# Kernel tuning notes

Measured on AMD Instinct MI355X. Metric: run time of the kernel, lower is better.

The kernel has to match this reference:

```python
import jax, jax.numpy as jnp
import numpy as np

B, S, D = 32, 2048, 64
DK, DV = 24, 32

def setup_inputs() -> dict:
    key = jax.random.key(0)
    ks = jax.random.split(key, 5)
    # PyTorch nn.Linear(in,out) weight is [out,in]; we store transposed [in,out]
    # so y = x @ W matches x @ weight.T. Kaiming-uniform-ish scale.
    def init(k, fan_in, shape):
        bound = 1.0 / np.sqrt(fan_in)
        return jax.random.uniform(k, shape, jnp.float32, -bound, bound)
    return {
        "x": jax.random.normal(ks[0], (B, S, D), jnp.float32),
        "Wq": init(ks[1], D, (D, DK)),
        "Wk": init(ks[2], D, (D, DK)),
        "Wv": init(ks[3], D, (D, DV)),
        "Wh": init(ks[4], DV, (DV, D)),
    }

def reference(x, Wq, Wk, Wv, Wh):
    # x: [B,S,64]
    q = jnp.einsum("bsd,dk->bsk", x, Wq)          # [B,S,24]
    k = jnp.einsum("bsd,dk->bsk", x, Wk)          # [B,S,24]
    v = jnp.einsum("bsd,dk->bsk", x, Wv)          # [B,S,32]
    a = jnp.einsum("bqk,btk->bqt", q, k)          # [B,S,S], q @ k^T
    # NOTE: softmax over dim=1 (the query axis), as in the original module.
    a = jax.nn.softmax(a, axis=1)
    h1 = jnp.einsum("bqt,btv->bqv", a, v)         # [B,S,32]
    return jnp.einsum("bqv,vd->bqd", h1, Wh)      # [B,S,64]
```

## Files before the change

kernel.cpp:

```cpp
#include <hip/hip_runtime.h>
#include <hip/hip_bf16.h>

#define NB 32
#define NS 2048
#define ND 64
#define NDK 24
#define NDV 32
#define LOG2E 1.4426950408889634f

typedef __attribute__((ext_vector_type(8))) short short8;
typedef __attribute__((ext_vector_type(4))) float f32x4;

typedef __attribute__((address_space(3))) unsigned int lds_u32;
typedef __attribute__((address_space(1))) const unsigned int glb_u32;

#define LFENCE asm volatile("" ::: "memory")

__device__ __forceinline__ void cp16(const void* g, void* l) {
  __builtin_amdgcn_global_load_lds((glb_u32*)g, (lds_u32*)l, 16, 0, 0);
}

__device__ __forceinline__ float fexp2(float x) {
  return __builtin_amdgcn_exp2f(x);
}

__device__ __forceinline__ unsigned pk2(float a, float b) {
  __hip_bfloat16 ha = __float2bfloat16(a), hb = __float2bfloat16(b);
  return ((unsigned)__builtin_bit_cast(unsigned short, hb) << 16) |
         (unsigned)__builtin_bit_cast(unsigned short, ha);
}

__device__ __forceinline__ unsigned pku(__hip_bfloat16 lo, __hip_bfloat16 hi) {
  return ((unsigned)__builtin_bit_cast(unsigned short, hi) << 16) |
         (unsigned)__builtin_bit_cast(unsigned short, lo);
}


__global__ __launch_bounds__(256) void prep_kernel(
    const float* __restrict__ Wq, const float* __restrict__ Wk,
    const float* __restrict__ Wv, const float* __restrict__ Wh,
    __hip_bfloat16* __restrict__ wt, __hip_bfloat16* __restrict__ whT) {
  const int tid = threadIdx.x;
  for (int o = tid; o < 6144; o += 256) {
    const int n = o / 72, d = o % 72;
    float val = 0.f;
    if (o < 5760 && d < ND) {
      if (n < 24)      val = Wq[d * NDK + n] * LOG2E;
      else if (n < 48) val = Wk[d * NDK + (n - 24)];
      else             val = Wv[d * NDV + (n - 48)];
    }
    wt[o] = __float2bfloat16(val);
  }
  {
    const int lane = tid & 63, l15 = lane & 15, lg = lane >> 4;
    const int d = (tid >> 6) * 16 + l15;
    uint4 u;
    u.x = pk2(Wh[(lg * 8 + 0) * ND + d], Wh[(lg * 8 + 1) * ND + d]);
    u.y = pk2(Wh[(lg * 8 + 2) * ND + d], Wh[(lg * 8 + 3) * ND + d]);
    u.z = pk2(Wh[(lg * 8 + 4) * ND + d], Wh[(lg * 8 + 5) * ND + d]);
    u.w = pk2(Wh[(lg * 8 + 6) * ND + d], Wh[(lg * 8 + 7) * ND + d]);
    ((uint4*)whT)[tid] = u;
  }
}

__global__ __launch_bounds__(256) void proj_kernel(
    const float* __restrict__ x, const __hip_bfloat16* __restrict__ wt,
    __hip_bfloat16* __restrict__ qfb, __hip_bfloat16* __restrict__ kfb,
    __hip_bfloat16* __restrict__ vfb) {
  __shared__ __hip_bfloat16 xsb[64 * 72];
  __shared__ __hip_bfloat16 Wt[6144];
  __shared__ __hip_bfloat16 os[64][81];

  const int tid = threadIdx.x;
  const size_t row0 = (size_t)blockIdx.x * 64;
  const int b = (int)(row0 >> 11);
  const int tile = (int)((row0 >> 6) & 31);
  const int wv = tid >> 6, lane = tid & 63;
  const int l15 = lane & 15, lg = lane >> 4;

  #pragma unroll
  for (int i = 0; i < 3; ++i)
    cp16((const char*)wt + (i * 256 + tid) * 16, (char*)Wt + (i * 256 + tid) * 16);

  {
    const int r = tid >> 2, c16 = (tid & 3) * 16;
    const float4* src = (const float4*)(x + (row0 + r) * ND + c16);
    unsigned u[8];
    #pragma unroll
    for (int i = 0; i < 4; ++i) {
      float4 f = src[i];
      u[2 * i] = pk2(f.x, f.y);
      u[2 * i + 1] = pk2(f.z, f.w);
    }
    uint4* dst = (uint4*)((char*)xsb + r * 144 + c16 * 2);
    dst[0] = make_uint4(u[0], u[1], u[2], u[3]);
    dst[1] = make_uint4(u[4], u[5], u[6], u[7]);
  }
  __syncthreads();

  {
    short8 a[2];
    #pragma unroll
    for (int kc = 0; kc < 2; ++kc)
      a[kc] = *(const short8*)((char*)xsb + ((wv * 16 + l15) * 72 + kc * 32 + lg * 8) * 2);
    const f32x4 z = {0.f, 0.f, 0.f, 0.f};
    #pragma unroll
    for (int nt = 0; nt < 5; ++nt) {
      f32x4 acc = z;
      #pragma unroll
      for (int kc = 0; kc < 2; ++kc) {
        const short8 bfr = *(const short8*)((char*)Wt + ((nt * 16 + l15) * 72 + kc * 32 + lg * 8) * 2);
        acc = __builtin_amdgcn_mfma_f32_16x16x32_bf16(a[kc], bfr, acc, 0, 0, 0);
      }
      #pragma unroll
      for (int r = 0; r < 4; ++r)
        os[wv * 16 + lg * 4 + r][nt * 16 + l15] = __float2bfloat16(acc[r]);
    }
  }
  __syncthreads();

  const size_t fbase = ((size_t)(b * 32 + tile)) * 4 * 256;
  for (int j = tid; j < 2048; j += 256) {
    const int arr = j >> 10, jj = j & 1023;
    const int qs = jj >> 8, ln = (jj >> 2) & 63, wd = jj & 3;
    const int row = qs * 16 + (ln & 15);
    const int c0 = (ln >> 4) * 8 + wd * 2;
    unsigned u = 0;
    if (c0 < 24) u = pku(os[row][arr * 24 + c0], os[row][arr * 24 + c0 + 1]);
    unsigned* dst = (unsigned*)(arr ? kfb : qfb);
    dst[fbase + (size_t)qs * 256 + ln * 4 + wd] = u;
  }
  for (int j = tid; j < 1024; j += 256) {
    const int fi = j >> 8;
    const int ln = (j >> 2) & 63, wd = j & 3;
    const int v = (fi & 1) * 16 + (ln & 15);
    const int tl = (fi >> 1) * 32 + (ln >> 4) * 8 + wd * 2;
    const unsigned u = pku(os[tl][48 + v], os[tl + 1][48 + v]);
    ((unsigned*)vfb)[fbase + (size_t)fi * 256 + ln * 4 + wd] = u;
  }
}

struct QT { short8 q0, q1, q2, q3; };

__device__ __forceinline__ void loadQ(QT& t, const __hip_bfloat16* qp, int it, int lane) {
  const __hip_bfloat16* p = qp + (size_t)it * 2048 + lane * 8;
  t.q0 = *(const short8*)(p);
  t.q1 = *(const short8*)(p + 512);
  t.q2 = *(const short8*)(p + 1024);
  t.q3 = *(const short8*)(p + 1536);
}

__device__ __forceinline__ void accQ(const QT& t, short8 kf0, short8 kf1,
                                     f32x4& s0, f32x4& s1) {
  const f32x4 z = {0.f, 0.f, 0.f, 0.f};
  #pragma unroll
  for (int qi = 0; qi < 4; ++qi) {
    const short8 q = qi == 0 ? t.q0 : qi == 1 ? t.q1 : qi == 2 ? t.q2 : t.q3;
    f32x4 d0 = __builtin_amdgcn_mfma_f32_16x16x32_bf16(kf0, q, z, 0, 0, 0);
    f32x4 d1 = __builtin_amdgcn_mfma_f32_16x16x32_bf16(kf1, q, z, 0, 0, 0);
    #pragma unroll
    for (int r = 0; r < 4; ++r) { s0[r] += fexp2(d0[r]); s1[r] += fexp2(d1[r]); }
  }
}

__global__ __launch_bounds__(256) void stats_kernel(
    const __hip_bfloat16* __restrict__ qfb, const __hip_bfloat16* __restrict__ kfb,
    float* __restrict__ ls) {
  const int g = blockIdx.x;
  const int xcd = g & 7, loc = g >> 3;
  const int b = (xcd << 2) + (loc >> 4);
  const int tg = loc & 15;
  const int tid = threadIdx.x;
  const int wv = tid >> 6, lane = tid & 63;
  const int l15 = lane & 15, lg = lane >> 4;
  const int tile_t = tg * 2 + (wv >> 1);
  const int ib = (wv & 1) * 2;

  short8 kf[2];
  #pragma unroll
  for (int j = 0; j < 2; ++j)
    kf[j] = *(const short8*)(kfb + (((size_t)(b * 32 + tile_t)) * 4 + ib + j) * 512 + lane * 8);

  const __hip_bfloat16* qp = qfb + (size_t)b * 32 * 2048;
  const f32x4 z = {0.f, 0.f, 0.f, 0.f};
  f32x4 s0 = z, s1 = z;

  QT A, B;
  loadQ(A, qp, 0, lane);
  for (int it2 = 0; it2 < 16; ++it2) {
    const int itA = it2 * 2;
    loadQ(B, qp, itA + 1, lane);
    accQ(A, kf[0], kf[1], s0, s1);
    loadQ(A, qp, itA + 2 < 32 ? itA + 2 : 31, lane);
    accQ(B, kf[0], kf[1], s0, s1);
  }
  #pragma unroll
  for (int m = 1; m < 16; m <<= 1) {
    #pragma unroll
    for (int r = 0; r < 4; ++r) {
      s0[r] += __shfl_xor(s0[r], m);
      s1[r] += __shfl_xor(s1[r], m);
    }
  }
  if (l15 == 0) {
    f32x4 o0, o1;
    #pragma unroll
    for (int r = 0; r < 4; ++r) { o0[r] = -__log2f(s0[r]); o1[r] = -__log2f(s1[r]); }
    float* lp = ls + ((size_t)b << 11) + tile_t * 64 + ib * 16 + lg * 4;
    *(f32x4*)(lp) = o0;
    *(f32x4*)(lp + 16) = o1;
  }
}

struct KVT {
  short8 k0, k1, k2, k3;
  short8 v0, v1, v2, v3;
  f32x4 l0, l1, l2, l3;
};

__device__ __forceinline__ void loadKV(KVT& t, const __hip_bfloat16* kp0,
    const __hip_bfloat16* vp0, const float* lsb, int it, int lane, int lg) {
  const __hip_bfloat16* kp = kp0 + (size_t)it * 2048 + lane * 8;
  t.k0 = *(const short8*)(kp);
  t.k1 = *(const short8*)(kp + 512);
  t.k2 = *(const short8*)(kp + 1024);
  t.k3 = *(const short8*)(kp + 1536);
  const __hip_bfloat16* vp = vp0 + (size_t)it * 2048 + lane * 8;
  t.v0 = *(const short8*)(vp);
  t.v1 = *(const short8*)(vp + 512);
  t.v2 = *(const short8*)(vp + 1024);
  t.v3 = *(const short8*)(vp + 1536);
  const float* lp = lsb + it * 64 + lg * 4;
  t.l0 = *(const f32x4*)(lp);
  t.l1 = *(const f32x4*)(lp + 16);
  t.l2 = *(const f32x4*)(lp + 32);
  t.l3 = *(const f32x4*)(lp + 48);
}

__device__ __forceinline__ void computeKV(const KVT& t, short8 qf, char* Pw,
                                          int lg, f32x4& h10, f32x4& h11) {
  f32x4 d;
  uint2 w;
  d = __builtin_amdgcn_mfma_f32_16x16x32_bf16(t.k0, qf, t.l0, 0, 0, 0);
  w.x = pk2(fexp2(d[0]), fexp2(d[1]));
  w.y = pk2(fexp2(d[2]), fexp2(d[3]));
  *(uint2*)(Pw + lg * 8) = w;
  d = __builtin_amdgcn_mfma_f32_16x16x32_bf16(t.k1, qf, t.l1, 0, 0, 0);
  w.x = pk2(fexp2(d[0]), fexp2(d[1]));
  w.y = pk2(fexp2(d[2]), fexp2(d[3]));
  *(uint2*)(Pw + 32 + lg * 8) = w;
  d = __builtin_amdgcn_mfma_f32_16x16x32_bf16(t.k2, qf, t.l2, 0, 0, 0);
  w.x = pk2(fexp2(d[0]), fexp2(d[1]));
  w.y = pk2(fexp2(d[2]), fexp2(d[3]));
  *(uint2*)(Pw + 64 + lg * 8) = w;
  d = __builtin_amdgcn_mfma_f32_16x16x32_bf16(t.k3, qf, t.l3, 0, 0, 0);
  w.x = pk2(fexp2(d[0]), fexp2(d[1]));
  w.y = pk2(fexp2(d[2]), fexp2(d[3]));
  *(uint2*)(Pw + 96 + lg * 8) = w;
  LFENCE;
  const short8 p0 = *(const short8*)(Pw + lg * 16);
  const short8 p1 = *(const short8*)(Pw + 64 + lg * 16);
  h10 = __builtin_amdgcn_mfma_f32_16x16x32_bf16(p0, t.v0, h10, 0, 0, 0);
  h11 = __builtin_amdgcn_mfma_f32_16x16x32_bf16(p0, t.v1, h11, 0, 0, 0);
  h10 = __builtin_amdgcn_mfma_f32_16x16x32_bf16(p1, t.v2, h10, 0, 0, 0);
  h11 = __builtin_amdgcn_mfma_f32_16x16x32_bf16(p1, t.v3, h11, 0, 0, 0);
  LFENCE;
}

__global__ __launch_bounds__(256) void attn_kernel(
    const __hip_bfloat16* __restrict__ qfb, const __hip_bfloat16* __restrict__ kfb,
    const __hip_bfloat16* __restrict__ vfb, const float* __restrict__ ls,
    const __hip_bfloat16* __restrict__ whT, float* __restrict__ out) {
  __shared__ char Ps[4 * 2816];

  const int g = blockIdx.x;
  const int xcd = g & 7, loc = g >> 3;
  const int b = (xcd << 2) + (loc >> 4);
  const int qg = loc & 15;
  const int tid = threadIdx.x;
  const int wv = tid >> 6, lane = tid & 63;
  const int l15 = lane & 15, lg = lane >> 4;
  const int tile_q = qg * 2 + (wv >> 1);
  const int ib = (wv & 1) * 2;

  char* Pw = Ps + wv * 2816 + l15 * 176;

  short8 qf[2];
  #pragma unroll
  for (int qi = 0; qi < 2; ++qi)
    qf[qi] = *(const short8*)(qfb + (((size_t)(b * 32 + tile_q)) * 4 + ib + qi) * 512 + lane * 8);

  const __hip_bfloat16* kp0 = kfb + (size_t)b * 32 * 2048;
  const __hip_bfloat16* vp0 = vfb + (size_t)b * 32 * 2048;
  const float* lsb = ls + ((size_t)b << 11);

  const f32x4 z = {0.f, 0.f, 0.f, 0.f};
  f32x4 h1[2][2] = {{z, z}, {z, z}};

  KVT A, B;
  loadKV(A, kp0, vp0, lsb, 0, lane, lg);
  for (int it2 = 0; it2 < 16; ++it2) {
    const int itA = it2 * 2;
    loadKV(B, kp0, vp0, lsb, itA + 1, lane, lg);
    computeKV(A, qf[0], Pw, lg, h1[0][0], h1[0][1]);
    computeKV(A, qf[1], Pw, lg, h1[1][0], h1[1][1]);
    loadKV(A, kp0, vp0, lsb, itA + 2 < 32 ? itA + 2 : 31, lane, lg);
    computeKV(B, qf[0], Pw, lg, h1[0][0], h1[0][1]);
    computeKV(B, qf[1], Pw, lg, h1[1][0], h1[1][1]);
  }

  short8 wf[4];
  #pragma unroll
  for (int dt = 0; dt < 4; ++dt)
    wf[dt] = *(const short8*)(whT + dt * 512 + lane * 8);
  #pragma unroll
  for (int qi = 0; qi < 2; ++qi) {
    #pragma unroll
    for (int vs = 0; vs < 2; ++vs)
      #pragma unroll
      for (int r = 0; r < 4; ++r)
        *(unsigned short*)(Ps + wv * 2816 + (lg * 4 + r) * 176 + (vs * 16 + l15) * 2) =
            __builtin_bit_cast(unsigned short, __float2bfloat16(h1[qi][vs][r]));
    LFENCE;
    const short8 hf = *(const short8*)(Pw + lg * 16);
    float* ob = out + (size_t)(b * NS + tile_q * 64 + (ib + qi) * 16 + lg * 4) * ND + l15;
    #pragma unroll
    for (int dt = 0; dt < 4; ++dt) {
      f32x4 o = __builtin_amdgcn_mfma_f32_16x16x32_bf16(hf, wf[dt], z, 0, 0, 0);
      float* op = ob + dt * 16;
      op[0] = o[0];
      op[ND] = o[1];
      op[2 * ND] = o[2];
      op[3 * ND] = o[3];
    }
    LFENCE;
  }
}

extern "C" void kernel_launch(void* const* d_in, const int* in_sizes, int n_in,
                              void* d_out, int out_size, void* d_ws, size_t ws_size,
                              hipStream_t stream) {
  const float* x  = (const float*)d_in[0];
  const float* Wq = (const float*)d_in[1];
  const float* Wk = (const float*)d_in[2];
  const float* Wv = (const float*)d_in[3];
  const float* Wh = (const float*)d_in[4];
  float* out = (float*)d_out;

  char* ws = (char*)d_ws;
  __hip_bfloat16* qfb = (__hip_bfloat16*)ws;
  __hip_bfloat16* kfb = (__hip_bfloat16*)(ws + 4194304);
  __hip_bfloat16* vfb = (__hip_bfloat16*)(ws + 8388608);
  float*          lsp = (float*)(ws + 12582912);
  __hip_bfloat16* whT = (__hip_bfloat16*)(ws + 12845056);
  __hip_bfloat16* wt  = (__hip_bfloat16*)(ws + 12849152);

  hipLaunchKernelGGL(prep_kernel, dim3(1), dim3(256), 0, stream,
                     Wq, Wk, Wv, Wh, wt, whT);
  hipLaunchKernelGGL(proj_kernel, dim3(1024), dim3(256), 0, stream,
                     x, wt, qfb, kfb, vfb);
  hipLaunchKernelGGL(stats_kernel, dim3(512), dim3(256), 0, stream,
                     qfb, kfb, lsp);
  hipLaunchKernelGGL(attn_kernel, dim3(512), dim3(256), 0, stream,
                     qfb, kfb, vfb, lsp, whT, out);
}
```

Baseline: 76.65 us.

## Software-pipeline QK exp and PV MFMA stages with double-buffered LDS P tiles

Splits the per-tile compute into separate QK+exp write, P read, and PV MFMA stages, and double-buffers the per-wave P scratch in LDS. The next QK/exp can then be issued while the previous P tile is read back and multiplied with V, hiding LDS round-trip latency and exp work behind MFMA. LDS use per block doubles and register pressure rises because more fragments are live, which may reduce occupancy. Loads of the next K/V tiles are also rescheduled within the loop.

```diff
diff --git a/kernel.cpp b/kernel.cpp
--- a/kernel.cpp
+++ b/kernel.cpp
@@ -237,33 +237,40 @@
   t.l3 = *(const f32x4*)(lp + 48);
 }
 
-__device__ __forceinline__ void computeKV(const KVT& t, short8 qf, char* Pw,
-                                          int lg, f32x4& h10, f32x4& h11) {
+__device__ __forceinline__ void qkw(const KVT& t, short8 qf, char* bufr, int lg) {
   f32x4 d;
   uint2 w;
   d = __builtin_amdgcn_mfma_f32_16x16x32_bf16(t.k0, qf, t.l0, 0, 0, 0);
   w.x = pk2(fexp2(d[0]), fexp2(d[1]));
   w.y = pk2(fexp2(d[2]), fexp2(d[3]));
-  *(uint2*)(Pw + lg * 8) = w;
+  *(uint2*)(bufr + lg * 8) = w;
   d = __builtin_amdgcn_mfma_f32_16x16x32_bf16(t.k1, qf, t.l1, 0, 0, 0);
   w.x = pk2(fexp2(d[0]), fexp2(d[1]));
   w.y = pk2(fexp2(d[2]), fexp2(d[3]));
-  *(uint2*)(Pw + 32 + lg * 8) = w;
+  *(uint2*)(bufr + 32 + lg * 8) = w;
   d = __builtin_amdgcn_mfma_f32_16x16x32_bf16(t.k2, qf, t.l2, 0, 0, 0);
   w.x = pk2(fexp2(d[0]), fexp2(d[1]));
   w.y = pk2(fexp2(d[2]), fexp2(d[3]));
-  *(uint2*)(Pw + 64 + lg * 8) = w;
+  *(uint2*)(bufr + 64 + lg * 8) = w;
   d = __builtin_amdgcn_mfma_f32_16x16x32_bf16(t.k3, qf, t.l3, 0, 0, 0);
   w.x = pk2(fexp2(d[0]), fexp2(d[1]));
   w.y = pk2(fexp2(d[2]), fexp2(d[3]));
-  *(uint2*)(Pw + 96 + lg * 8) = w;
+  *(uint2*)(bufr + 96 + lg * 8) = w;
   LFENCE;
-  const short8 p0 = *(const short8*)(Pw + lg * 16);
-  const short8 p1 = *(const short8*)(Pw + 64 + lg * 16);
-  h10 = __builtin_amdgcn_mfma_f32_16x16x32_bf16(p0, t.v0, h10, 0, 0, 0);
-  h11 = __builtin_amdgcn_mfma_f32_16x16x32_bf16(p0, t.v1, h11, 0, 0, 0);
-  h10 = __builtin_amdgcn_mfma_f32_16x16x32_bf16(p1, t.v2, h10, 0, 0, 0);
-  h11 = __builtin_amdgcn_mfma_f32_16x16x32_bf16(p1, t.v3, h11, 0, 0, 0);
+}
+
+__device__ __forceinline__ void prd(const char* bufr, int lg, short8& p0, short8& p1) {
+  p0 = *(const short8*)(bufr + lg * 16);
+  p1 = *(const short8*)(bufr + 64 + lg * 16);
+  LFENCE;
+}
+
+__device__ __forceinline__ void pvm(const KVT& t, short8 p0, short8 p1,
+                                    f32x4& ha, f32x4& hb) {
+  ha = __builtin_amdgcn_mfma_f32_16x16x32_bf16(p0, t.v0, ha, 0, 0, 0);
+  hb = __builtin_amdgcn_mfma_f32_16x16x32_bf16(p0, t.v1, hb, 0, 0, 0);
+  ha = __builtin_amdgcn_mfma_f32_16x16x32_bf16(p1, t.v2, ha, 0, 0, 0);
+  hb = __builtin_amdgcn_mfma_f32_16x16x32_bf16(p1, t.v3, hb, 0, 0, 0);
   LFENCE;
 }
 
@@ -271,7 +278,7 @@
     const __hip_bfloat16* __restrict__ qfb, const __hip_bfloat16* __restrict__ kfb,
     const __hip_bfloat16* __restrict__ vfb, const float* __restrict__ ls,
     const __hip_bfloat16* __restrict__ whT, float* __restrict__ out) {
-  __shared__ char Ps[4 * 2816];
+  __shared__ char Ps[4 * 2 * 2816];
 
   const int g = blockIdx.x;
   const int xcd = g & 7, loc = g >> 3;
@@ -283,7 +290,8 @@
   const int tile_q = qg * 2 + (wv >> 1);
   const int ib = (wv & 1) * 2;
 
-  char* Pw = Ps + wv * 2816 + l15 * 176;
+  char* buf0 = Ps + wv * 5632 + l15 * 176;
+  char* buf1 = buf0 + 2816;
 
   short8 qf[2];
   #pragma unroll
@@ -299,30 +307,43 @@
 
   KVT A, B;
   loadKV(A, kp0, vp0, lsb, 0, lane, lg);
-  for (int it2 = 0; it2 < 16; ++it2) {
-    const int itA = it2 * 2;
-    loadKV(B, kp0, vp0, lsb, itA + 1, lane, lg);
-    computeKV(A, qf[0], Pw, lg, h1[0][0], h1[0][1]);
-    computeKV(A, qf[1], Pw, lg, h1[1][0], h1[1][1]);
-    loadKV(A, kp0, vp0, lsb, itA + 2 < 32 ? itA + 2 : 31, lane, lg);
-    computeKV(B, qf[0], Pw, lg, h1[0][0], h1[0][1]);
-    computeKV(B, qf[1], Pw, lg, h1[1][0], h1[1][1]);
+  loadKV(B, kp0, vp0, lsb, 1, lane, lg);
+  qkw(A, qf[0], buf0, lg);
+
+  short8 p0, p1;
+  for (int j = 0; j < 16; ++j) {
+    const int t2 = 2 * j;
+    prd(buf0, lg, p0, p1);
+    qkw(A, qf[1], buf1, lg);
+    pvm(A, p0, p1, h1[0][0], h1[0][1]);
+    prd(buf1, lg, p0, p1);
+    qkw(B, qf[0], buf0, lg);
+    pvm(A, p0, p1, h1[1][0], h1[1][1]);
+    if (j < 15) loadKV(A, kp0, vp0, lsb, t2 + 2, lane, lg);
+    prd(buf0, lg, p0, p1);
+    qkw(B, qf[1], buf1, lg);
+    pvm(B, p0, p1, h1[0][0], h1[0][1]);
+    prd(buf1, lg, p0, p1);
+    if (j < 15) qkw(A, qf[0], buf0, lg);
+    pvm(B, p0, p1, h1[1][0], h1[1][1]);
+    if (j < 15) loadKV(B, kp0, vp0, lsb, t2 + 3, lane, lg);
   }
 
   short8 wf[4];
   #pragma unroll
   for (int dt = 0; dt < 4; ++dt)
     wf[dt] = *(const short8*)(whT + dt * 512 + lane * 8);
+  char* Pregion = Ps + wv * 5632;
   #pragma unroll
   for (int qi = 0; qi < 2; ++qi) {
     #pragma unroll
     for (int vs = 0; vs < 2; ++vs)
       #pragma unroll
       for (int r = 0; r < 4; ++r)
-        *(unsigned short*)(Ps + wv * 2816 + (lg * 4 + r) * 176 + (vs * 16 + l15) * 2) =
+        *(unsigned short*)(Pregion + (lg * 4 + r) * 176 + (vs * 16 + l15) * 2) =
             __builtin_bit_cast(unsigned short, __float2bfloat16(h1[qi][vs][r]));
     LFENCE;
-    const short8 hf = *(const short8*)(Pw + lg * 16);
+    const short8 hf = *(const short8*)(buf0 + lg * 16);
     float* ob = out + (size_t)(b * NS + tile_q * 64 + (ib + qi) * 16 + lg * 4) * ND + l15;
     #pragma unroll
     for (int dt = 0; dt < 4; ++dt) {
```

Result: no change. 78.08 us (+1.9%).
